# Kernel optimization log

Hardware: AMD Instinct MI355X
Metric: run time of the kernel (lower is better)

The kernel has to match this reference:

```python
import jax, jax.numpy as jnp
import numpy as np

H, HD = 8, 32            # num_heads, head_dim
OUT = H * HD             # out_channels = 256
NUM_GRAPHS = 1


def segment_softmax(logits, seg, num_segments):
    m = jax.ops.segment_max(logits, seg, num_segments=num_segments)
    m = jnp.where(jnp.isfinite(m), m, 0.0)
    e = jnp.exp(logits - m[seg])
    s = jax.ops.segment_sum(e, seg, num_segments=num_segments)
    return e / (s[seg] + 1e-16)


def setup_inputs():
    key = jax.random.key(0)
    ks = jax.random.split(key, 16)
    N, E, IN = 30000, 600000, 128
    s = 0.05
    return {
        "x": jax.random.normal(ks[0], (N, IN), jnp.float32),
        "edge_index": jax.random.randint(ks[1], (2, E), 0, N, jnp.int32),
        "edge_attr": jax.random.normal(ks[2], (E,), jnp.float32),
        "batch": jnp.zeros((N,), jnp.int32),
        # per-head GATConv params (stacked over heads)
        "W": jax.random.normal(ks[3], (H, IN, HD), jnp.float32) * s,
        "a_src": jax.random.normal(ks[4], (H, HD), jnp.float32) * s,
        "a_dst": jax.random.normal(ks[5], (H, HD), jnp.float32) * s,
        "conv_b": jnp.zeros((H, HD), jnp.float32),
        # shared fc (used twice in forward)
        "fc_w": jax.random.normal(ks[6], (OUT, OUT), jnp.float32) * s,
        "fc_b": jnp.zeros((OUT,), jnp.float32),
        "ln_w": jnp.ones((OUT,), jnp.float32),
        "ln_b": jnp.zeros((OUT,), jnp.float32),
        "gate_w": jax.random.normal(ks[7], (1, OUT), jnp.float32) * s,
        "gate_b": jnp.zeros((1,), jnp.float32),
        "gfc_w": jax.random.normal(ks[8], (OUT, OUT), jnp.float32) * s,
        "gfc_b": jnp.zeros((OUT,), jnp.float32),
    }


def reference(x, edge_index, edge_attr, batch, W, a_src, a_dst, conv_b,
              fc_w, fc_b, ln_w, ln_b, gate_w, gate_b, gfc_w, gfc_b):
    N = x.shape[0]
    # (dropout p=0.2 is identity in eval mode)
    # --- multi-head GATConv (heads=1 each, vectorized over H); PyG default
    # add_self_loops=True; edge_dim=None so edge_attr is ignored by the conv.
    loops = jnp.arange(N, dtype=edge_index.dtype)
    src = jnp.concatenate([edge_index[0], loops])  # [Etot]
    dst = jnp.concatenate([edge_index[1], loops])
    xp = jnp.einsum('ni,hid->nhd', x, W)                    # [N,H,HD]
    alpha_src = jnp.sum(xp * a_src[None], axis=-1)          # [N,H]
    alpha_dst = jnp.sum(xp * a_dst[None], axis=-1)          # [N,H]
    logits = jax.nn.leaky_relu(alpha_src[src] + alpha_dst[dst], 0.2)  # [Etot,H]
    alpha = segment_softmax(logits, dst, N)                 # [Etot,H]
    msg = alpha[:, :, None] * xp[src]                        # [Etot,H,HD]
    out = jax.ops.segment_sum(msg, dst, num_segments=N) + conv_b[None]
    x_local = out.reshape(N, OUT)                            # concat over heads
    # --- dense re-attention / softmax fusion
    sa = jax.nn.softmax(jax.nn.leaky_relu(x_local @ fc_w.T + fc_b, 0.01), axis=-1)
    x_local = jax.nn.leaky_relu(x_local * sa, 0.2)
    x_local = x_local @ fc_w.T + fc_b
    # LayerNorm (eps=1e-5)
    mu = jnp.mean(x_local, axis=-1, keepdims=True)
    var = jnp.mean(jnp.square(x_local - mu), axis=-1, keepdims=True)
    x_local = (x_local - mu) / jnp.sqrt(var + 1e-5) * ln_w + ln_b
    # F.normalize(p=2, dim=1)
    nrm = jnp.sqrt(jnp.sum(jnp.square(x_local), axis=1, keepdims=True))
    x_local = x_local / jnp.maximum(nrm, 1e-12)
    # --- GlobalAttention pooling
    gate = (x_local @ gate_w.T + gate_b)[:, 0]               # [N]
    g = segment_softmax(gate, batch, NUM_GRAPHS)             # [N]
    x_global = jax.ops.segment_sum(g[:, None] * x_local, batch,
                                   num_segments=NUM_GRAPHS)  # [1,OUT]
    ga = jax.nn.softmax(jax.nn.relu(x_global @ gfc_w.T + gfc_b), axis=-1)
    return x_local * ga[batch]                               # [N,OUT]
```

## Files before the change

kernel.cpp:

```cpp
#include <hip/hip_runtime.h>


#define PAD 64
#define CSTR 16

typedef __attribute__((ext_vector_type(8))) short bf16x8;
typedef __attribute__((ext_vector_type(4))) float f32x4;

__device__ __forceinline__ float leaky_f(float v, float s) { return v > 0.f ? v : s * v; }
__device__ __forceinline__ unsigned short f2bf(float f) {
  unsigned int u = __float_as_uint(f);
  u += 0x7fffu + ((u >> 16) & 1u);
  return (unsigned short)(u >> 16);
}
__device__ __forceinline__ float bf2f(unsigned short u) {
  return __uint_as_float(((unsigned int)u) << 16);
}
__device__ __forceinline__ float bf_lo(unsigned int u) {
  return __uint_as_float(u << 16);
}
__device__ __forceinline__ float bf_hi(unsigned int u) {
  return __uint_as_float(u & 0xffff0000u);
}
__device__ __forceinline__ float red16_sum(float v) {
#pragma unroll
  for (int m = 1; m < 16; m <<= 1) v += __shfl_xor(v, m);
  return v;
}
__device__ __forceinline__ float red16_max(float v) {
#pragma unroll
  for (int m = 1; m < 16; m <<= 1) v = fmaxf(v, __shfl_xor(v, m));
  return v;
}

__global__ void repack_zero_kernel(const float* __restrict__ W, const float* __restrict__ fc_w,
                                   const float* __restrict__ gfc_w,
                                   unsigned short* __restrict__ Wb,
                                   unsigned short* __restrict__ fcB, float* __restrict__ gfcT,
                                   int* __restrict__ count, int n) {
  int i = blockIdx.x * 256 + threadIdx.x;
  if (i < 256 * 128) {
    int c = i >> 7, k = i & 127;
    Wb[i] = f2bf(W[((c >> 5) * 128 + k) * 32 + (c & 31)]);
  } else if (i < 256 * 128 + 256 * 256) {
    int j = i - 256 * 128;
    fcB[j] = f2bf(fc_w[j]);
  } else if (i < 256 * 128 + 2 * 256 * 256) {
    int j = i - 256 * 128 - 256 * 256;
    gfcT[j] = gfc_w[(j & 255) * 256 + (j >> 8)];
  }
  if (i < n) count[i * CSTR] = 0;
}

template <int A_BF16>
__device__ __forceinline__ void gemm_body_64x256(
    const void* __restrict__ Av, const unsigned short* __restrict__ B,
    int row0, int n_rows, int K, short As[64][72], short Bs[256][72],
    f32x4 acc[4][4]) {
  int t = threadIdx.x;
  int wave = t >> 6, lane = t & 63;
  int m16 = lane & 15, quad = lane >> 4;
  int wc = wave * 64;
  for (int k0 = 0; k0 < K; k0 += 64) {
    if (A_BF16) {
      const unsigned short* A = (const unsigned short*)Av;
#pragma unroll
      for (int p = 0; p < 2; ++p) {
        int e = (p * 256 + t) * 8;
        int row = e >> 6, k = e & 63;
        int ar = row0 + row; if (ar > n_rows - 1) ar = n_rows - 1;
        uint4 q = *(const uint4*)(A + (size_t)ar * K + k0 + k);
        *(uint4*)&As[row][k] = q;
      }
    } else {
      const float* A = (const float*)Av;
#pragma unroll
      for (int p = 0; p < 4; ++p) {
        int e = (p * 256 + t) * 4;
        int row = e >> 6, k = e & 63;
        int ar = row0 + row; if (ar > n_rows - 1) ar = n_rows - 1;
        float4 q = *(const float4*)(A + (size_t)ar * K + k0 + k);
        unsigned int lo = (unsigned int)f2bf(q.x) | ((unsigned int)f2bf(q.y) << 16);
        unsigned int hi = (unsigned int)f2bf(q.z) | ((unsigned int)f2bf(q.w) << 16);
        *(uint2*)&As[row][k] = make_uint2(lo, hi);
      }
    }
#pragma unroll
    for (int p = 0; p < 8; ++p) {
      int e = (p * 256 + t) * 8;
      int nn = e >> 6, k = e & 63;
      uint4 q = *(const uint4*)(B + (size_t)nn * K + k0 + k);
      *(uint4*)&Bs[nn][k] = q;
    }
    __syncthreads();
#pragma unroll
    for (int ks = 0; ks < 64; ks += 32) {
      bf16x8 af[4], bfr[4];
#pragma unroll
      for (int i = 0; i < 4; ++i)
        af[i] = *(const bf16x8*)&As[i * 16 + m16][ks + quad * 8];
#pragma unroll
      for (int j = 0; j < 4; ++j)
        bfr[j] = *(const bf16x8*)&Bs[wc + j * 16 + m16][ks + quad * 8];
#pragma unroll
      for (int i = 0; i < 4; ++i)
#pragma unroll
        for (int j = 0; j < 4; ++j)
          acc[i][j] = __builtin_amdgcn_mfma_f32_16x16x32_bf16(af[i], bfr[j], acc[i][j], 0, 0, 0);
    }
    __syncthreads();
  }
}

__global__ __launch_bounds__(256) void gemm_xp_scatter(
    const float* __restrict__ A, const unsigned short* __restrict__ B,
    const float* __restrict__ a_src, const float* __restrict__ a_dst,
    unsigned short* __restrict__ xpb, float* __restrict__ asrc,
    float* __restrict__ adst, int n_rows,
    const int* __restrict__ esrc, const int* __restrict__ edst,
    int* __restrict__ count, unsigned short* __restrict__ ssrc, int E,
    int scat_blocks) {
  __shared__ short As[64][72];
  __shared__ short Bs[256][72];
  if ((int)blockIdx.x < scat_blocks) {
    int base = ((int)blockIdx.x * 256 + threadIdx.x) * 4;
    if (base + 4 <= E) {
      int4 d4 = *(const int4*)(edst + base);
      int4 s4 = *(const int4*)(esrc + base);
      int p0 = atomicAdd(&count[d4.x * CSTR], 1);
      int p1 = atomicAdd(&count[d4.y * CSTR], 1);
      int p2 = atomicAdd(&count[d4.z * CSTR], 1);
      int p3 = atomicAdd(&count[d4.w * CSTR], 1);
      if (p0 < PAD) ssrc[(size_t)d4.x * PAD + p0] = (unsigned short)s4.x;
      if (p1 < PAD) ssrc[(size_t)d4.y * PAD + p1] = (unsigned short)s4.y;
      if (p2 < PAD) ssrc[(size_t)d4.z * PAD + p2] = (unsigned short)s4.z;
      if (p3 < PAD) ssrc[(size_t)d4.w * PAD + p3] = (unsigned short)s4.w;
    } else {
      for (int i = base; i < E; ++i) {
        int d = edst[i];
        int p = atomicAdd(&count[d * CSTR], 1);
        if (p < PAD) ssrc[(size_t)d * PAD + p] = (unsigned short)esrc[i];
      }
    }
    return;
  }
  int t = threadIdx.x;
  int wave = t >> 6, lane = t & 63;
  int m16 = lane & 15, quad = lane >> 4;
  int wc = wave * 64;
  int row0 = ((int)blockIdx.x - scat_blocks) * 64;
  f32x4 acc[4][4];
#pragma unroll
  for (int i = 0; i < 4; ++i)
#pragma unroll
    for (int j = 0; j < 4; ++j) acc[i][j] = (f32x4){0.f, 0.f, 0.f, 0.f};
  gemm_body_64x256<0>(A, B, row0, n_rows, 128, As, Bs, acc);

  float av[4], bd[4];
#pragma unroll
  for (int j = 0; j < 4; ++j) {
    int c = wc + j * 16 + m16;
    av[j] = a_src[c];
    bd[j] = a_dst[c];
  }
#pragma unroll
  for (int i = 0; i < 4; ++i)
#pragma unroll
    for (int v = 0; v < 4; ++v) {
      int r = row0 + i * 16 + quad * 4 + v;
      if (r < n_rows) {
#pragma unroll
        for (int j = 0; j < 4; ++j)
          xpb[(size_t)r * 256 + wc + j * 16 + m16] = f2bf(acc[i][j][v]);
      }
      float s0 = acc[i][0][v] * av[0] + acc[i][1][v] * av[1];
      float s1 = acc[i][2][v] * av[2] + acc[i][3][v] * av[3];
      float d0 = acc[i][0][v] * bd[0] + acc[i][1][v] * bd[1];
      float d1 = acc[i][2][v] * bd[2] + acc[i][3][v] * bd[3];
      s0 = red16_sum(s0); s1 = red16_sum(s1);
      d0 = red16_sum(d0); d1 = red16_sum(d1);
      if (m16 == 0 && r < n_rows) {
        asrc[(size_t)r * 8 + 2 * wave] = s0;
        asrc[(size_t)r * 8 + 2 * wave + 1] = s1;
        adst[(size_t)r * 8 + 2 * wave] = d0;
        adst[(size_t)r * 8 + 2 * wave + 1] = d1;
      }
    }
}

__global__ __launch_bounds__(256) void agg_kernel(
    const unsigned short* __restrict__ xpb, const float* __restrict__ asrc,
    const float* __restrict__ adst, const int* __restrict__ count,
    const unsigned short* __restrict__ ssrc, const float* __restrict__ conv_b,
    unsigned short* __restrict__ xlocb, int n_nodes) {
  int t = threadIdx.x;
  int lane = t & 63;
  int hl = lane & 31;
  int half = lane >> 5;
  int wv = t >> 6;
  int n = blockIdx.x * 8 + wv * 2 + half;
  bool active = n < n_nodes;
  int nn = active ? n : 0;
  int hc = hl >> 2;
  int hp = hl & 7;
  int up = hl >> 3;
  int srcbase = (half << 5) + hc;

  float ad_p = adst[nn * 8 + hp];
  float ad_c = adst[nn * 8 + hc];

  float p = __expf(leaky_f(asrc[nn * 8 + hc] + ad_c, 0.2f));
  uint4 q = *(const uint4*)(xpb + (size_t)nn * 256 + hl * 8);
  float acc[8];
  acc[0] = p * bf_lo(q.x); acc[1] = p * bf_hi(q.x);
  acc[2] = p * bf_lo(q.y); acc[3] = p * bf_hi(q.y);
  acc[4] = p * bf_lo(q.z); acc[5] = p * bf_hi(q.z);
  acc[6] = p * bf_lo(q.w); acc[7] = p * bf_hi(q.w);
  float ssum = p;

  int beg = nn * PAD;
  int end = beg + (active ? count[nn * CSTR] : 0);
  int j = beg;
  for (; j + 4 <= end; j += 4) {
    ushort4 s4 = *(const ushort4*)(ssrc + j);
    int svp = (up & 1) ? ((up & 2) ? s4.w : s4.y) : ((up & 2) ? s4.z : s4.x);
    float pp = __expf(leaky_f(asrc[svp * 8 + hp] + ad_p, 0.2f));
    uint4 q0 = *(const uint4*)(xpb + (size_t)s4.x * 256 + hl * 8);
    uint4 q1 = *(const uint4*)(xpb + (size_t)s4.y * 256 + hl * 8);
    uint4 q2 = *(const uint4*)(xpb + (size_t)s4.z * 256 + hl * 8);
    uint4 q3 = *(const uint4*)(xpb + (size_t)s4.w * 256 + hl * 8);
    float p0 = __shfl(pp, srcbase);
    float p1 = __shfl(pp, srcbase + 8);
    float p2 = __shfl(pp, srcbase + 16);
    float p3 = __shfl(pp, srcbase + 24);
    acc[0] += p0 * bf_lo(q0.x); acc[1] += p0 * bf_hi(q0.x);
    acc[2] += p0 * bf_lo(q0.y); acc[3] += p0 * bf_hi(q0.y);
    acc[4] += p0 * bf_lo(q0.z); acc[5] += p0 * bf_hi(q0.z);
    acc[6] += p0 * bf_lo(q0.w); acc[7] += p0 * bf_hi(q0.w);
    acc[0] += p1 * bf_lo(q1.x); acc[1] += p1 * bf_hi(q1.x);
    acc[2] += p1 * bf_lo(q1.y); acc[3] += p1 * bf_hi(q1.y);
    acc[4] += p1 * bf_lo(q1.z); acc[5] += p1 * bf_hi(q1.z);
    acc[6] += p1 * bf_lo(q1.w); acc[7] += p1 * bf_hi(q1.w);
    acc[0] += p2 * bf_lo(q2.x); acc[1] += p2 * bf_hi(q2.x);
    acc[2] += p2 * bf_lo(q2.y); acc[3] += p2 * bf_hi(q2.y);
    acc[4] += p2 * bf_lo(q2.z); acc[5] += p2 * bf_hi(q2.z);
    acc[6] += p2 * bf_lo(q2.w); acc[7] += p2 * bf_hi(q2.w);
    acc[0] += p3 * bf_lo(q3.x); acc[1] += p3 * bf_hi(q3.x);
    acc[2] += p3 * bf_lo(q3.y); acc[3] += p3 * bf_hi(q3.y);
    acc[4] += p3 * bf_lo(q3.z); acc[5] += p3 * bf_hi(q3.z);
    acc[6] += p3 * bf_lo(q3.w); acc[7] += p3 * bf_hi(q3.w);
    ssum += p0 + p1 + p2 + p3;
  }
  for (; j < end; ++j) {
    int sv = ssrc[j];
    float p1 = __expf(leaky_f(asrc[sv * 8 + hc] + ad_c, 0.2f));
    uint4 q1 = *(const uint4*)(xpb + (size_t)sv * 256 + hl * 8);
    acc[0] += p1 * bf_lo(q1.x); acc[1] += p1 * bf_hi(q1.x);
    acc[2] += p1 * bf_lo(q1.y); acc[3] += p1 * bf_hi(q1.y);
    acc[4] += p1 * bf_lo(q1.z); acc[5] += p1 * bf_hi(q1.z);
    acc[6] += p1 * bf_lo(q1.w); acc[7] += p1 * bf_hi(q1.w);
    ssum += p1;
  }
  if (!active) return;
  float inv = 1.f / (ssum + 1e-16f);
  float4 b0 = *(const float4*)(conv_b + hl * 8);
  float4 b1 = *(const float4*)(conv_b + hl * 8 + 4);
  unsigned int w0 = (unsigned int)f2bf(acc[0] * inv + b0.x) |
                    ((unsigned int)f2bf(acc[1] * inv + b0.y) << 16);
  unsigned int w1 = (unsigned int)f2bf(acc[2] * inv + b0.z) |
                    ((unsigned int)f2bf(acc[3] * inv + b0.w) << 16);
  unsigned int w2 = (unsigned int)f2bf(acc[4] * inv + b1.x) |
                    ((unsigned int)f2bf(acc[5] * inv + b1.y) << 16);
  unsigned int w3 = (unsigned int)f2bf(acc[6] * inv + b1.z) |
                    ((unsigned int)f2bf(acc[7] * inv + b1.w) << 16);
  *(uint4*)(xlocb + (size_t)n * 256 + hl * 8) = make_uint4(w0, w1, w2, w3);
}

__global__ __launch_bounds__(256) void gemm_sm(
    const unsigned short* __restrict__ A, const unsigned short* __restrict__ B,
    const float* __restrict__ bias, unsigned short* __restrict__ x2b, int n_rows) {
  __shared__ short As[64][72];
  __shared__ short Bs[256][72];
  __shared__ float red[4][64];
  __shared__ float rowv[64];
  int t = threadIdx.x;
  int wave = t >> 6, lane = t & 63;
  int m16 = lane & 15, quad = lane >> 4;
  int wc = wave * 64;
  int row0 = blockIdx.x * 64;
  f32x4 acc[4][4];
#pragma unroll
  for (int i = 0; i < 4; ++i)
#pragma unroll
    for (int j = 0; j < 4; ++j) acc[i][j] = (f32x4){0.f, 0.f, 0.f, 0.f};
  gemm_body_64x256<1>(A, B, row0, n_rows, 256, As, Bs, acc);

  float bvv[4];
#pragma unroll
  for (int j = 0; j < 4; ++j) bvv[j] = bias[wc + j * 16 + m16];
#pragma unroll
  for (int i = 0; i < 4; ++i)
#pragma unroll
    for (int j = 0; j < 4; ++j)
#pragma unroll
      for (int v = 0; v < 4; ++v)
        acc[i][j][v] = leaky_f(acc[i][j][v] + bvv[j], 0.01f);

  float M[4][4];
#pragma unroll
  for (int i = 0; i < 4; ++i)
#pragma unroll
    for (int v = 0; v < 4; ++v) {
      float m = fmaxf(fmaxf(acc[i][0][v], acc[i][1][v]), fmaxf(acc[i][2][v], acc[i][3][v]));
      M[i][v] = red16_max(m);
    }
  if (m16 == 0)
#pragma unroll
    for (int i = 0; i < 4; ++i)
#pragma unroll
      for (int v = 0; v < 4; ++v) red[wave][i * 16 + quad * 4 + v] = M[i][v];
  __syncthreads();
  if (t < 64) rowv[t] = fmaxf(fmaxf(red[0][t], red[1][t]), fmaxf(red[2][t], red[3][t]));
  __syncthreads();
#pragma unroll
  for (int i = 0; i < 4; ++i)
#pragma unroll
    for (int v = 0; v < 4; ++v) M[i][v] = rowv[i * 16 + quad * 4 + v];
  __syncthreads();

  float S[4][4];
#pragma unroll
  for (int i = 0; i < 4; ++i)
#pragma unroll
    for (int v = 0; v < 4; ++v) {
#pragma unroll
      for (int j = 0; j < 4; ++j) acc[i][j][v] = __expf(acc[i][j][v] - M[i][v]);
      float s = acc[i][0][v] + acc[i][1][v] + acc[i][2][v] + acc[i][3][v];
      S[i][v] = red16_sum(s);
    }
  if (m16 == 0)
#pragma unroll
    for (int i = 0; i < 4; ++i)
#pragma unroll
      for (int v = 0; v < 4; ++v) red[wave][i * 16 + quad * 4 + v] = S[i][v];
  __syncthreads();
  if (t < 64) rowv[t] = red[0][t] + red[1][t] + red[2][t] + red[3][t];
  __syncthreads();

#pragma unroll
  for (int i = 0; i < 4; ++i)
#pragma unroll
    for (int v = 0; v < 4; ++v) {
      int r = row0 + i * 16 + quad * 4 + v;
      float inv = 1.f / rowv[i * 16 + quad * 4 + v];
      if (r < n_rows) {
#pragma unroll
        for (int j = 0; j < 4; ++j) {
          int c = wc + j * 16 + m16;
          float xv = bf2f(A[(size_t)r * 256 + c]);
          x2b[(size_t)r * 256 + c] = f2bf(leaky_f(xv * acc[i][j][v] * inv, 0.2f));
        }
      }
    }
}

__global__ __launch_bounds__(256) void gemm_ln(
    const unsigned short* __restrict__ A, const unsigned short* __restrict__ B,
    const float* __restrict__ bias, const float* __restrict__ ln_w,
    const float* __restrict__ ln_b, const float* __restrict__ gate_w,
    const float* __restrict__ gate_b, unsigned short* __restrict__ Cout,
    float* __restrict__ pooled, float* __restrict__ pooledS, int n_rows) {
  __shared__ short As[64][72];
  __shared__ short Bs[256][72];
  __shared__ float red[4][64];
  __shared__ float rowv[64];
  __shared__ float eg[64];
  int t = threadIdx.x;
  int wave = t >> 6, lane = t & 63;
  int m16 = lane & 15, quad = lane >> 4;
  int wc = wave * 64;
  int row0 = blockIdx.x * 64;
  f32x4 acc[4][4];
#pragma unroll
  for (int i = 0; i < 4; ++i)
#pragma unroll
    for (int j = 0; j < 4; ++j) acc[i][j] = (f32x4){0.f, 0.f, 0.f, 0.f};
  gemm_body_64x256<1>(A, B, row0, n_rows, 256, As, Bs, acc);

  float bvv[4], lw[4], lb[4], gw[4];
#pragma unroll
  for (int j = 0; j < 4; ++j) {
    int c = wc + j * 16 + m16;
    bvv[j] = bias[c]; lw[j] = ln_w[c]; lb[j] = ln_b[c]; gw[j] = gate_w[c];
  }
#pragma unroll
  for (int i = 0; i < 4; ++i)
#pragma unroll
    for (int j = 0; j < 4; ++j)
#pragma unroll
      for (int v = 0; v < 4; ++v) acc[i][j][v] += bvv[j];

  float MU[4][4];
#pragma unroll
  for (int i = 0; i < 4; ++i)
#pragma unroll
    for (int v = 0; v < 4; ++v)
      MU[i][v] = red16_sum(acc[i][0][v] + acc[i][1][v] + acc[i][2][v] + acc[i][3][v]);
  if (m16 == 0)
#pragma unroll
    for (int i = 0; i < 4; ++i)
#pragma unroll
      for (int v = 0; v < 4; ++v) red[wave][i * 16 + quad * 4 + v] = MU[i][v];
  __syncthreads();
  if (t < 64) rowv[t] = (red[0][t] + red[1][t] + red[2][t] + red[3][t]) * (1.f / 256.f);
  __syncthreads();
#pragma unroll
  for (int i = 0; i < 4; ++i)
#pragma unroll
    for (int v = 0; v < 4; ++v) MU[i][v] = rowv[i * 16 + quad * 4 + v];
  __syncthreads();
#pragma unroll
  for (int i = 0; i < 4; ++i)
#pragma unroll
    for (int j = 0; j < 4; ++j)
#pragma unroll
      for (int v = 0; v < 4; ++v) acc[i][j][v] -= MU[i][v];

  float RS[4][4];
#pragma unroll
  for (int i = 0; i < 4; ++i)
#pragma unroll
    for (int v = 0; v < 4; ++v) {
      float q = acc[i][0][v] * acc[i][0][v] + acc[i][1][v] * acc[i][1][v] +
                acc[i][2][v] * acc[i][2][v] + acc[i][3][v] * acc[i][3][v];
      RS[i][v] = red16_sum(q);
    }
  if (m16 == 0)
#pragma unroll
    for (int i = 0; i < 4; ++i)
#pragma unroll
      for (int v = 0; v < 4; ++v) red[wave][i * 16 + quad * 4 + v] = RS[i][v];
  __syncthreads();
  if (t < 64)
    rowv[t] = rsqrtf((red[0][t] + red[1][t] + red[2][t] + red[3][t]) * (1.f / 256.f) + 1e-5f);
  __syncthreads();
#pragma unroll
  for (int i = 0; i < 4; ++i)
#pragma unroll
    for (int v = 0; v < 4; ++v) RS[i][v] = rowv[i * 16 + quad * 4 + v];
  __syncthreads();
#pragma unroll
  for (int i = 0; i < 4; ++i)
#pragma unroll
    for (int j = 0; j < 4; ++j)
#pragma unroll
      for (int v = 0; v < 4; ++v)
        acc[i][j][v] = acc[i][j][v] * RS[i][v] * lw[j] + lb[j];

  float NV[4][4];
#pragma unroll
  for (int i = 0; i < 4; ++i)
#pragma unroll
    for (int v = 0; v < 4; ++v) {
      float q = acc[i][0][v] * acc[i][0][v] + acc[i][1][v] * acc[i][1][v] +
                acc[i][2][v] * acc[i][2][v] + acc[i][3][v] * acc[i][3][v];
      NV[i][v] = red16_sum(q);
    }
  if (m16 == 0)
#pragma unroll
    for (int i = 0; i < 4; ++i)
#pragma unroll
      for (int v = 0; v < 4; ++v) red[wave][i * 16 + quad * 4 + v] = NV[i][v];
  __syncthreads();
  if (t < 64)
    rowv[t] = 1.f / fmaxf(sqrtf(red[0][t] + red[1][t] + red[2][t] + red[3][t]), 1e-12f);
  __syncthreads();
#pragma unroll
  for (int i = 0; i < 4; ++i)
#pragma unroll
    for (int v = 0; v < 4; ++v) NV[i][v] = rowv[i * 16 + quad * 4 + v];
  __syncthreads();
#pragma unroll
  for (int i = 0; i < 4; ++i)
#pragma unroll
    for (int j = 0; j < 4; ++j)
#pragma unroll
      for (int v = 0; v < 4; ++v) acc[i][j][v] *= NV[i][v];

  float GP[4][4];
#pragma unroll
  for (int i = 0; i < 4; ++i)
#pragma unroll
    for (int v = 0; v < 4; ++v) {
      float g = acc[i][0][v] * gw[0] + acc[i][1][v] * gw[1] +
                acc[i][2][v] * gw[2] + acc[i][3][v] * gw[3];
      GP[i][v] = red16_sum(g);
    }
  if (m16 == 0)
#pragma unroll
    for (int i = 0; i < 4; ++i)
#pragma unroll
      for (int v = 0; v < 4; ++v) red[wave][i * 16 + quad * 4 + v] = GP[i][v];
  __syncthreads();
  if (t < 64) {
    float gp = red[0][t] + red[1][t] + red[2][t] + red[3][t];
    float e = (row0 + t < n_rows) ? __expf(gp + gate_b[0]) : 0.f;
    eg[t] = e;
#pragma unroll
    for (int m = 1; m < 64; m <<= 1) e += __shfl_xor(e, m);
    if (t == 0) pooledS[blockIdx.x] = e;
  }
  __syncthreads();

  {
    float pt[4] = {0.f, 0.f, 0.f, 0.f};
#pragma unroll
    for (int i = 0; i < 4; ++i)
#pragma unroll
      for (int v = 0; v < 4; ++v) {
        float w = eg[i * 16 + quad * 4 + v];
#pragma unroll
        for (int j = 0; j < 4; ++j) pt[j] += w * acc[i][j][v];
      }
#pragma unroll
    for (int j = 0; j < 4; ++j) {
      float sj = pt[j];
      sj += __shfl_xor(sj, 16);
      sj += __shfl_xor(sj, 32);
      if (quad == 0) pooled[(size_t)blockIdx.x * 256 + wc + j * 16 + m16] = sj;
    }
  }

#pragma unroll
  for (int i = 0; i < 4; ++i)
#pragma unroll
    for (int v = 0; v < 4; ++v) {
      int r = row0 + i * 16 + quad * 4 + v;
      if (r < n_rows) {
#pragma unroll
        for (int j = 0; j < 4; ++j)
          Cout[(size_t)r * 256 + wc + j * 16 + m16] = f2bf(acc[i][j][v]);
      }
    }
}

__global__ __launch_bounds__(1024) void finalize_gfc(
    const float* __restrict__ pooled, const float* __restrict__ pooledS, int nb,
    const float* __restrict__ gfcT, const float* __restrict__ gfc_b,
    float* __restrict__ ga) {
  __shared__ float sm[1024];
  __shared__ float xs[256];
  __shared__ float av[256];
  int t = threadIdx.x, c = t & 255, part = t >> 8;
  float s = 0.f;
  for (int b = t; b < nb; b += 1024) s += pooledS[b];
  sm[t] = s;
  __syncthreads();
  for (int st = 512; st > 0; st >>= 1) {
    if (t < st) sm[t] += sm[t + st];
    __syncthreads();
  }
  float S = sm[0];
  __syncthreads();
  float xc = 0.f;
#pragma unroll 4
  for (int b = part; b < nb; b += 4) xc += pooled[(size_t)b * 256 + c];
  sm[t] = xc;
  __syncthreads();
  if (part == 0) xs[c] = (sm[c] + sm[c + 256] + sm[c + 512] + sm[c + 768]) / (S + 1e-16f);
  __syncthreads();
  float a = 0.f;
  for (int i = part * 64; i < part * 64 + 64; ++i) a += xs[i] * gfcT[i * 256 + c];
  sm[t] = a;
  __syncthreads();
  if (part == 0)
    av[c] = fmaxf(sm[c] + sm[c + 256] + sm[c + 512] + sm[c + 768] + gfc_b[c], 0.f);
  __syncthreads();
  sm[t] = (t < 256) ? av[t] : -1e30f;
  __syncthreads();
  for (int st = 512; st > 0; st >>= 1) {
    if (t < st) sm[t] = fmaxf(sm[t], sm[t + st]);
    __syncthreads();
  }
  float m = sm[0];
  __syncthreads();
  if (part == 0) av[c] = __expf(av[c] - m);
  __syncthreads();
  sm[t] = (t < 256) ? av[t] : 0.f;
  __syncthreads();
  for (int st = 512; st > 0; st >>= 1) {
    if (t < st) sm[t] += sm[t + st];
    __syncthreads();
  }
  if (part == 0) ga[c] = av[c] / sm[0];
}

__global__ void out_kernel(const ushort4* __restrict__ xlb4, const float4* __restrict__ ga4,
                           float4* __restrict__ out4, int total4) {
  int i = blockIdx.x * 256 + threadIdx.x;
  if (i >= total4) return;
  ushort4 q = xlb4[i];
  float4 g = ga4[i & 63];
  float4 v;
  v.x = bf2f(q.x) * g.x; v.y = bf2f(q.y) * g.y;
  v.z = bf2f(q.z) * g.z; v.w = bf2f(q.w) * g.w;
  out4[i] = v;
}

extern "C" void kernel_launch(void* const* d_in, const int* in_sizes, int n_in,
                              void* d_out, int out_size, void* d_ws, size_t ws_size,
                              hipStream_t stream) {
  const float* x      = (const float*)d_in[0];
  const int* edge_idx = (const int*)d_in[1];
  const float* W      = (const float*)d_in[4];
  const float* a_src  = (const float*)d_in[5];
  const float* a_dst  = (const float*)d_in[6];
  const float* conv_b = (const float*)d_in[7];
  const float* fc_w   = (const float*)d_in[8];
  const float* fc_b   = (const float*)d_in[9];
  const float* ln_w   = (const float*)d_in[10];
  const float* ln_b   = (const float*)d_in[11];
  const float* gate_w = (const float*)d_in[12];
  const float* gate_b = (const float*)d_in[13];
  const float* gfc_w  = (const float*)d_in[14];
  const float* gfc_b  = (const float*)d_in[15];
  (void)n_in; (void)out_size; (void)ws_size;

  int N = in_sizes[0] / 128;
  int E = in_sizes[1] / 2;
  const int* src = edge_idx;
  const int* dst = edge_idx + E;

  char* p = (char*)d_ws;
  auto alloc = [&](size_t bytes) -> char* {
    char* r = p;
    p += (bytes + 255) & ~(size_t)255;
    return r;
  };
  int g64 = (N + 63) / 64;
  unsigned short* xlocb = (unsigned short*)alloc((size_t)N * 256 * 2);
  unsigned short* xpb  = (unsigned short*)alloc((size_t)N * 256 * 2);
  unsigned short* x2b  = (unsigned short*)alloc((size_t)N * 256 * 2);
  unsigned short* xlb  = (unsigned short*)alloc((size_t)N * 256 * 2);
  float* asrc  = (float*)alloc((size_t)N * 8 * 4);
  float* adst  = (float*)alloc((size_t)N * 8 * 4);
  unsigned short* Wb   = (unsigned short*)alloc(256 * 128 * 2);
  unsigned short* fcB  = (unsigned short*)alloc(256 * 256 * 2);
  float* gfcT  = (float*)alloc(256 * 256 * 4);
  int*   count = (int*)alloc((size_t)N * CSTR * 4);
  unsigned short* ssrc = (unsigned short*)alloc((size_t)N * PAD * 2);
  float* pooled  = (float*)alloc((size_t)g64 * 256 * 4);
  float* pooledS = (float*)alloc((size_t)g64 * 4);
  float* ga    = (float*)alloc(1024);

  int eb4 = (E + 1023) / 1024;

  repack_zero_kernel<<<(256 * 128 + 2 * 256 * 256 + 255) / 256, 256, 0, stream>>>(
      W, fc_w, gfc_w, Wb, fcB, gfcT, count, N);
  gemm_xp_scatter<<<eb4 + g64, 256, 0, stream>>>(
      x, Wb, a_src, a_dst, xpb, asrc, adst, N, src, dst, count, ssrc, E, eb4);
  agg_kernel<<<(N + 7) / 8, 256, 0, stream>>>(
      xpb, asrc, adst, count, ssrc, conv_b, xlocb, N);
  gemm_sm<<<g64, 256, 0, stream>>>(xlocb, fcB, fc_b, x2b, N);
  gemm_ln<<<g64, 256, 0, stream>>>(x2b, fcB, fc_b, ln_w, ln_b, gate_w, gate_b,
                                   xlb, pooled, pooledS, N);
  finalize_gfc<<<1, 1024, 0, stream>>>(pooled, pooledS, g64, gfcT, gfc_b, ga);
  out_kernel<<<(N * 64 + 255) / 256, 256, 0, stream>>>(
      (const ushort4*)xlb, (const float4*)ga, (float4*)d_out, N * 64);
}
```

Baseline: 248.3 us.

## Fuse softmax-reattention GEMM with LayerNorm GEMM and prefetch neighbor indices in aggregation

Merges the two fc GEMM kernels into one. The whole 64x256 row tile of the aggregated features stays in shared memory, and the reattention output is rewritten in place, so the intermediate x2b buffer is never written to or read back from global memory and one launch goes away. The aggregation loop also software-prefetches the next group of four source indices and their attention logits, which shortens the dependent load chain. The cost is a larger shared-memory footprint per block (about 33KB for X2 plus Bs), which may lower occupancy.

```diff
diff --git a/kernel.cpp b/kernel.cpp
--- a/kernel.cpp
+++ b/kernel.cpp
@@ -31,6 +31,9 @@
 #pragma unroll
   for (int m = 1; m < 16; m <<= 1) v = fmaxf(v, __shfl_xor(v, m));
   return v;
+}
+__device__ __forceinline__ int pick4(ushort4 s, int up) {
+  return (up & 1) ? ((up & 2) ? s.w : s.y) : ((up & 2) ? s.z : s.x);
 }
 
 __global__ void repack_zero_kernel(const float* __restrict__ W, const float* __restrict__ fc_w,
@@ -52,9 +55,8 @@
   if (i < n) count[i * CSTR] = 0;
 }
 
-template <int A_BF16>
-__device__ __forceinline__ void gemm_body_64x256(
-    const void* __restrict__ Av, const unsigned short* __restrict__ B,
+__device__ __forceinline__ void gemm_body_f32(
+    const float* __restrict__ A, const unsigned short* __restrict__ B,
     int row0, int n_rows, int K, short As[64][72], short Bs[256][72],
     f32x4 acc[4][4]) {
   int t = threadIdx.x;
@@ -62,28 +64,15 @@
   int m16 = lane & 15, quad = lane >> 4;
   int wc = wave * 64;
   for (int k0 = 0; k0 < K; k0 += 64) {
-    if (A_BF16) {
-      const unsigned short* A = (const unsigned short*)Av;
-#pragma unroll
-      for (int p = 0; p < 2; ++p) {
-        int e = (p * 256 + t) * 8;
-        int row = e >> 6, k = e & 63;
-        int ar = row0 + row; if (ar > n_rows - 1) ar = n_rows - 1;
-        uint4 q = *(const uint4*)(A + (size_t)ar * K + k0 + k);
-        *(uint4*)&As[row][k] = q;
-      }
-    } else {
-      const float* A = (const float*)Av;
-#pragma unroll
-      for (int p = 0; p < 4; ++p) {
-        int e = (p * 256 + t) * 4;
-        int row = e >> 6, k = e & 63;
-        int ar = row0 + row; if (ar > n_rows - 1) ar = n_rows - 1;
-        float4 q = *(const float4*)(A + (size_t)ar * K + k0 + k);
-        unsigned int lo = (unsigned int)f2bf(q.x) | ((unsigned int)f2bf(q.y) << 16);
-        unsigned int hi = (unsigned int)f2bf(q.z) | ((unsigned int)f2bf(q.w) << 16);
-        *(uint2*)&As[row][k] = make_uint2(lo, hi);
-      }
+#pragma unroll
+    for (int p = 0; p < 4; ++p) {
+      int e = (p * 256 + t) * 4;
+      int row = e >> 6, k = e & 63;
+      int ar = row0 + row; if (ar > n_rows - 1) ar = n_rows - 1;
+      float4 q = *(const float4*)(A + (size_t)ar * K + k0 + k);
+      unsigned int lo = (unsigned int)f2bf(q.x) | ((unsigned int)f2bf(q.y) << 16);
+      unsigned int hi = (unsigned int)f2bf(q.z) | ((unsigned int)f2bf(q.w) << 16);
+      *(uint2*)&As[row][k] = make_uint2(lo, hi);
     }
 #pragma unroll
     for (int p = 0; p < 8; ++p) {
@@ -154,7 +143,7 @@
   for (int i = 0; i < 4; ++i)
 #pragma unroll
     for (int j = 0; j < 4; ++j) acc[i][j] = (f32x4){0.f, 0.f, 0.f, 0.f};
-  gemm_body_64x256<0>(A, B, row0, n_rows, 128, As, Bs, acc);
+  gemm_body_f32(A, B, row0, n_rows, 128, As, Bs, acc);
 
   float av[4], bd[4];
 #pragma unroll
@@ -218,38 +207,45 @@
   acc[6] = p * bf_lo(q.w); acc[7] = p * bf_hi(q.w);
   float ssum = p;
 
+  int cnt = active ? count[nn * CSTR] : 0;
   int beg = nn * PAD;
-  int end = beg + (active ? count[nn * CSTR] : 0);
+  int end = beg + cnt;
+  int jend = beg + (cnt & ~3);
   int j = beg;
-  for (; j + 4 <= end; j += 4) {
+  if (j < jend) {
     ushort4 s4 = *(const ushort4*)(ssrc + j);
-    int svp = (up & 1) ? ((up & 2) ? s4.w : s4.y) : ((up & 2) ? s4.z : s4.x);
-    float pp = __expf(leaky_f(asrc[svp * 8 + hp] + ad_p, 0.2f));
-    uint4 q0 = *(const uint4*)(xpb + (size_t)s4.x * 256 + hl * 8);
-    uint4 q1 = *(const uint4*)(xpb + (size_t)s4.y * 256 + hl * 8);
-    uint4 q2 = *(const uint4*)(xpb + (size_t)s4.z * 256 + hl * 8);
-    uint4 q3 = *(const uint4*)(xpb + (size_t)s4.w * 256 + hl * 8);
-    float p0 = __shfl(pp, srcbase);
-    float p1 = __shfl(pp, srcbase + 8);
-    float p2 = __shfl(pp, srcbase + 16);
-    float p3 = __shfl(pp, srcbase + 24);
-    acc[0] += p0 * bf_lo(q0.x); acc[1] += p0 * bf_hi(q0.x);
-    acc[2] += p0 * bf_lo(q0.y); acc[3] += p0 * bf_hi(q0.y);
-    acc[4] += p0 * bf_lo(q0.z); acc[5] += p0 * bf_hi(q0.z);
-    acc[6] += p0 * bf_lo(q0.w); acc[7] += p0 * bf_hi(q0.w);
-    acc[0] += p1 * bf_lo(q1.x); acc[1] += p1 * bf_hi(q1.x);
-    acc[2] += p1 * bf_lo(q1.y); acc[3] += p1 * bf_hi(q1.y);
-    acc[4] += p1 * bf_lo(q1.z); acc[5] += p1 * bf_hi(q1.z);
-    acc[6] += p1 * bf_lo(q1.w); acc[7] += p1 * bf_hi(q1.w);
-    acc[0] += p2 * bf_lo(q2.x); acc[1] += p2 * bf_hi(q2.x);
-    acc[2] += p2 * bf_lo(q2.y); acc[3] += p2 * bf_hi(q2.y);
-    acc[4] += p2 * bf_lo(q2.z); acc[5] += p2 * bf_hi(q2.z);
-    acc[6] += p2 * bf_lo(q2.w); acc[7] += p2 * bf_hi(q2.w);
-    acc[0] += p3 * bf_lo(q3.x); acc[1] += p3 * bf_hi(q3.x);
-    acc[2] += p3 * bf_lo(q3.y); acc[3] += p3 * bf_hi(q3.y);
-    acc[4] += p3 * bf_lo(q3.z); acc[5] += p3 * bf_hi(q3.z);
-    acc[6] += p3 * bf_lo(q3.w); acc[7] += p3 * bf_hi(q3.w);
-    ssum += p0 + p1 + p2 + p3;
+    float a_cur = asrc[pick4(s4, up) * 8 + hp];
+    for (; j < jend; j += 4) {
+      ushort4 s4n = (j + 4 < jend) ? *(const ushort4*)(ssrc + j + 4) : s4;
+      uint4 q0 = *(const uint4*)(xpb + (size_t)s4.x * 256 + hl * 8);
+      uint4 q1 = *(const uint4*)(xpb + (size_t)s4.y * 256 + hl * 8);
+      uint4 q2 = *(const uint4*)(xpb + (size_t)s4.z * 256 + hl * 8);
+      uint4 q3 = *(const uint4*)(xpb + (size_t)s4.w * 256 + hl * 8);
+      float pp = __expf(leaky_f(a_cur + ad_p, 0.2f));
+      float a_nxt = asrc[pick4(s4n, up) * 8 + hp];
+      float p0 = __shfl(pp, srcbase);
+      float p1 = __shfl(pp, srcbase + 8);
+      float p2 = __shfl(pp, srcbase + 16);
+      float p3 = __shfl(pp, srcbase + 24);
+      acc[0] += p0 * bf_lo(q0.x); acc[1] += p0 * bf_hi(q0.x);
+      acc[2] += p0 * bf_lo(q0.y); acc[3] += p0 * bf_hi(q0.y);
+      acc[4] += p0 * bf_lo(q0.z); acc[5] += p0 * bf_hi(q0.z);
+      acc[6] += p0 * bf_lo(q0.w); acc[7] += p0 * bf_hi(q0.w);
+      acc[0] += p1 * bf_lo(q1.x); acc[1] += p1 * bf_hi(q1.x);
+      acc[2] += p1 * bf_lo(q1.y); acc[3] += p1 * bf_hi(q1.y);
+      acc[4] += p1 * bf_lo(q1.z); acc[5] += p1 * bf_hi(q1.z);
+      acc[6] += p1 * bf_lo(q1.w); acc[7] += p1 * bf_hi(q1.w);
+      acc[0] += p2 * bf_lo(q2.x); acc[1] += p2 * bf_hi(q2.x);
+      acc[2] += p2 * bf_lo(q2.y); acc[3] += p2 * bf_hi(q2.y);
+      acc[4] += p2 * bf_lo(q2.z); acc[5] += p2 * bf_hi(q2.z);
+      acc[6] += p2 * bf_lo(q2.w); acc[7] += p2 * bf_hi(q2.w);
+      acc[0] += p3 * bf_lo(q3.x); acc[1] += p3 * bf_hi(q3.x);
+      acc[2] += p3 * bf_lo(q3.y); acc[3] += p3 * bf_hi(q3.y);
+      acc[4] += p3 * bf_lo(q3.z); acc[5] += p3 * bf_hi(q3.z);
+      acc[6] += p3 * bf_lo(q3.w); acc[7] += p3 * bf_hi(q3.w);
+      ssum += p0 + p1 + p2 + p3;
+      s4 = s4n; a_cur = a_nxt;
+    }
   }
   for (; j < end; ++j) {
     int sv = ssrc[j];
@@ -276,101 +272,13 @@
   *(uint4*)(xlocb + (size_t)n * 256 + hl * 8) = make_uint4(w0, w1, w2, w3);
 }
 
-__global__ __launch_bounds__(256) void gemm_sm(
-    const unsigned short* __restrict__ A, const unsigned short* __restrict__ B,
-    const float* __restrict__ bias, unsigned short* __restrict__ x2b, int n_rows) {
-  __shared__ short As[64][72];
-  __shared__ short Bs[256][72];
-  __shared__ float red[4][64];
-  __shared__ float rowv[64];
-  int t = threadIdx.x;
-  int wave = t >> 6, lane = t & 63;
-  int m16 = lane & 15, quad = lane >> 4;
-  int wc = wave * 64;
-  int row0 = blockIdx.x * 64;
-  f32x4 acc[4][4];
-#pragma unroll
-  for (int i = 0; i < 4; ++i)
-#pragma unroll
-    for (int j = 0; j < 4; ++j) acc[i][j] = (f32x4){0.f, 0.f, 0.f, 0.f};
-  gemm_body_64x256<1>(A, B, row0, n_rows, 256, As, Bs, acc);
-
-  float bvv[4];
-#pragma unroll
-  for (int j = 0; j < 4; ++j) bvv[j] = bias[wc + j * 16 + m16];
-#pragma unroll
-  for (int i = 0; i < 4; ++i)
-#pragma unroll
-    for (int j = 0; j < 4; ++j)
-#pragma unroll
-      for (int v = 0; v < 4; ++v)
-        acc[i][j][v] = leaky_f(acc[i][j][v] + bvv[j], 0.01f);
-
-  float M[4][4];
-#pragma unroll
-  for (int i = 0; i < 4; ++i)
-#pragma unroll
-    for (int v = 0; v < 4; ++v) {
-      float m = fmaxf(fmaxf(acc[i][0][v], acc[i][1][v]), fmaxf(acc[i][2][v], acc[i][3][v]));
-      M[i][v] = red16_max(m);
-    }
-  if (m16 == 0)
-#pragma unroll
-    for (int i = 0; i < 4; ++i)
-#pragma unroll
-      for (int v = 0; v < 4; ++v) red[wave][i * 16 + quad * 4 + v] = M[i][v];
-  __syncthreads();
-  if (t < 64) rowv[t] = fmaxf(fmaxf(red[0][t], red[1][t]), fmaxf(red[2][t], red[3][t]));
-  __syncthreads();
-#pragma unroll
-  for (int i = 0; i < 4; ++i)
-#pragma unroll
-    for (int v = 0; v < 4; ++v) M[i][v] = rowv[i * 16 + quad * 4 + v];
-  __syncthreads();
-
-  float S[4][4];
-#pragma unroll
-  for (int i = 0; i < 4; ++i)
-#pragma unroll
-    for (int v = 0; v < 4; ++v) {
-#pragma unroll
-      for (int j = 0; j < 4; ++j) acc[i][j][v] = __expf(acc[i][j][v] - M[i][v]);
-      float s = acc[i][0][v] + acc[i][1][v] + acc[i][2][v] + acc[i][3][v];
-      S[i][v] = red16_sum(s);
-    }
-  if (m16 == 0)
-#pragma unroll
-    for (int i = 0; i < 4; ++i)
-#pragma unroll
-      for (int v = 0; v < 4; ++v) red[wave][i * 16 + quad * 4 + v] = S[i][v];
-  __syncthreads();
-  if (t < 64) rowv[t] = red[0][t] + red[1][t] + red[2][t] + red[3][t];
-  __syncthreads();
-
-#pragma unroll
-  for (int i = 0; i < 4; ++i)
-#pragma unroll
-    for (int v = 0; v < 4; ++v) {
-      int r = row0 + i * 16 + quad * 4 + v;
-      float inv = 1.f / rowv[i * 16 + quad * 4 + v];
-      if (r < n_rows) {
-#pragma unroll
-        for (int j = 0; j < 4; ++j) {
-          int c = wc + j * 16 + m16;
-          float xv = bf2f(A[(size_t)r * 256 + c]);
-          x2b[(size_t)r * 256 + c] = f2bf(leaky_f(xv * acc[i][j][v] * inv, 0.2f));
-        }
-      }
-    }
-}
-
-__global__ __launch_bounds__(256) void gemm_ln(
+__global__ __launch_bounds__(256) void gemm_sm_ln(
     const unsigned short* __restrict__ A, const unsigned short* __restrict__ B,
     const float* __restrict__ bias, const float* __restrict__ ln_w,
     const float* __restrict__ ln_b, const float* __restrict__ gate_w,
     const float* __restrict__ gate_b, unsigned short* __restrict__ Cout,
     float* __restrict__ pooled, float* __restrict__ pooledS, int n_rows) {
-  __shared__ short As[64][72];
+  __shared__ short X2[64][260];
   __shared__ short Bs[256][72];
   __shared__ float red[4][64];
   __shared__ float rowv[64];
@@ -380,14 +288,147 @@
   int m16 = lane & 15, quad = lane >> 4;
   int wc = wave * 64;
   int row0 = blockIdx.x * 64;
+
+#pragma unroll
+  for (int p = 0; p < 8; ++p) {
+    int e = (p * 256 + t) * 8;
+    int row = e >> 8, col = e & 255;
+    int ar = row0 + row; if (ar > n_rows - 1) ar = n_rows - 1;
+    uint4 qv = *(const uint4*)(A + (size_t)ar * 256 + col);
+    *(uint4*)&X2[row][col] = qv;
+  }
+
   f32x4 acc[4][4];
 #pragma unroll
   for (int i = 0; i < 4; ++i)
 #pragma unroll
     for (int j = 0; j < 4; ++j) acc[i][j] = (f32x4){0.f, 0.f, 0.f, 0.f};
-  gemm_body_64x256<1>(A, B, row0, n_rows, 256, As, Bs, acc);
-
-  float bvv[4], lw[4], lb[4], gw[4];
+
+  for (int k0 = 0; k0 < 256; k0 += 64) {
+#pragma unroll
+    for (int p = 0; p < 8; ++p) {
+      int e = (p * 256 + t) * 8;
+      int nn = e >> 6, k = e & 63;
+      uint4 qv = *(const uint4*)(B + (size_t)nn * 256 + k0 + k);
+      *(uint4*)&Bs[nn][k] = qv;
+    }
+    __syncthreads();
+#pragma unroll
+    for (int ks = 0; ks < 64; ks += 32) {
+      bf16x8 af[4], bfr[4];
+#pragma unroll
+      for (int i = 0; i < 4; ++i)
+        af[i] = *(const bf16x8*)&X2[i * 16 + m16][k0 + ks + quad * 8];
+#pragma unroll
+      for (int j = 0; j < 4; ++j)
+        bfr[j] = *(const bf16x8*)&Bs[wc + j * 16 + m16][ks + quad * 8];
+#pragma unroll
+      for (int i = 0; i < 4; ++i)
+#pragma unroll
+        for (int j = 0; j < 4; ++j)
+          acc[i][j] = __builtin_amdgcn_mfma_f32_16x16x32_bf16(af[i], bfr[j], acc[i][j], 0, 0, 0);
+    }
+    __syncthreads();
+  }
+
+  float bvv[4];
+#pragma unroll
+  for (int j = 0; j < 4; ++j) bvv[j] = bias[wc + j * 16 + m16];
+#pragma unroll
+  for (int i = 0; i < 4; ++i)
+#pragma unroll
+    for (int j = 0; j < 4; ++j)
+#pragma unroll
+      for (int v = 0; v < 4; ++v)
+        acc[i][j][v] = leaky_f(acc[i][j][v] + bvv[j], 0.01f);
+
+  float M[4][4];
+#pragma unroll
+  for (int i = 0; i < 4; ++i)
+#pragma unroll
+    for (int v = 0; v < 4; ++v) {
+      float m = fmaxf(fmaxf(acc[i][0][v], acc[i][1][v]), fmaxf(acc[i][2][v], acc[i][3][v]));
+      M[i][v] = red16_max(m);
+    }
+  if (m16 == 0)
+#pragma unroll
+    for (int i = 0; i < 4; ++i)
+#pragma unroll
+      for (int v = 0; v < 4; ++v) red[wave][i * 16 + quad * 4 + v] = M[i][v];
+  __syncthreads();
+  if (t < 64) rowv[t] = fmaxf(fmaxf(red[0][t], red[1][t]), fmaxf(red[2][t], red[3][t]));
+  __syncthreads();
+#pragma unroll
+  for (int i = 0; i < 4; ++i)
+#pragma unroll
+    for (int v = 0; v < 4; ++v) M[i][v] = rowv[i * 16 + quad * 4 + v];
+  __syncthreads();
+
+  float S[4][4];
+#pragma unroll
+  for (int i = 0; i < 4; ++i)
+#pragma unroll
+    for (int v = 0; v < 4; ++v) {
+#pragma unroll
+      for (int j = 0; j < 4; ++j) acc[i][j][v] = __expf(acc[i][j][v] - M[i][v]);
+      float s = acc[i][0][v] + acc[i][1][v] + acc[i][2][v] + acc[i][3][v];
+      S[i][v] = red16_sum(s);
+    }
+  if (m16 == 0)
+#pragma unroll
+    for (int i = 0; i < 4; ++i)
+#pragma unroll
+      for (int v = 0; v < 4; ++v) red[wave][i * 16 + quad * 4 + v] = S[i][v];
+  __syncthreads();
+  if (t < 64) rowv[t] = red[0][t] + red[1][t] + red[2][t] + red[3][t];
+  __syncthreads();
+
+#pragma unroll
+  for (int i = 0; i < 4; ++i)
+#pragma unroll
+    for (int v = 0; v < 4; ++v) {
+      int rl = i * 16 + quad * 4 + v;
+      float inv = 1.f / rowv[rl];
+#pragma unroll
+      for (int j = 0; j < 4; ++j) {
+        int c = wc + j * 16 + m16;
+        float xv = bf2f((unsigned short)X2[rl][c]);
+        X2[rl][c] = (short)f2bf(leaky_f(xv * acc[i][j][v] * inv, 0.2f));
+      }
+    }
+
+#pragma unroll
+  for (int i = 0; i < 4; ++i)
+#pragma unroll
+    for (int j = 0; j < 4; ++j) acc[i][j] = (f32x4){0.f, 0.f, 0.f, 0.f};
+  for (int k0 = 0; k0 < 256; k0 += 64) {
+#pragma unroll
+    for (int p = 0; p < 8; ++p) {
+      int e = (p * 256 + t) * 8;
+      int nn = e >> 6, k = e & 63;
+      uint4 qv = *(const uint4*)(B + (size_t)nn * 256 + k0 + k);
+      *(uint4*)&Bs[nn][k] = qv;
+    }
+    __syncthreads();
+#pragma unroll
+    for (int ks = 0; ks < 64; ks += 32) {
+      bf16x8 af[4], bfr[4];
+#pragma unroll
+      for (int i = 0; i < 4; ++i)
+        af[i] = *(const bf16x8*)&X2[i * 16 + m16][k0 + ks + quad * 8];
+#pragma unroll
+      for (int j = 0; j < 4; ++j)
+        bfr[j] = *(const bf16x8*)&Bs[wc + j * 16 + m16][ks + quad * 8];
+#pragma unroll
+      for (int i = 0; i < 4; ++i)
+#pragma unroll
+        for (int j = 0; j < 4; ++j)
+          acc[i][j] = __builtin_amdgcn_mfma_f32_16x16x32_bf16(af[i], bfr[j], acc[i][j], 0, 0, 0);
+    }
+    __syncthreads();
+  }
+
+  float lw[4], lb[4], gw[4];
 #pragma unroll
   for (int j = 0; j < 4; ++j) {
     int c = wc + j * 16 + m16;
@@ -431,9 +472,9 @@
   for (int i = 0; i < 4; ++i)
 #pragma unroll
     for (int v = 0; v < 4; ++v) {
-      float q = acc[i][0][v] * acc[i][0][v] + acc[i][1][v] * acc[i][1][v] +
-                acc[i][2][v] * acc[i][2][v] + acc[i][3][v] * acc[i][3][v];
-      RS[i][v] = red16_sum(q);
+      float qq = acc[i][0][v] * acc[i][0][v] + acc[i][1][v] * acc[i][1][v] +
+                 acc[i][2][v] * acc[i][2][v] + acc[i][3][v] * acc[i][3][v];
+      RS[i][v] = red16_sum(qq);
     }
   if (m16 == 0)
 #pragma unroll
@@ -462,9 +503,9 @@
   for (int i = 0; i < 4; ++i)
 #pragma unroll
     for (int v = 0; v < 4; ++v) {
-      float q = acc[i][0][v] * acc[i][0][v] + acc[i][1][v] * acc[i][1][v] +
-                acc[i][2][v] * acc[i][2][v] + acc[i][3][v] * acc[i][3][v];
-      NV[i][v] = red16_sum(q);
+      float qq = acc[i][0][v] * acc[i][0][v] + acc[i][1][v] * acc[i][1][v] +
+                 acc[i][2][v] * acc[i][2][v] + acc[i][3][v] * acc[i][3][v];
+      NV[i][v] = red16_sum(qq);
     }
   if (m16 == 0)
 #pragma unroll
@@ -640,7 +681,6 @@
   int g64 = (N + 63) / 64;
   unsigned short* xlocb = (unsigned short*)alloc((size_t)N * 256 * 2);
   unsigned short* xpb  = (unsigned short*)alloc((size_t)N * 256 * 2);
-  unsigned short* x2b  = (unsigned short*)alloc((size_t)N * 256 * 2);
   unsigned short* xlb  = (unsigned short*)alloc((size_t)N * 256 * 2);
   float* asrc  = (float*)alloc((size_t)N * 8 * 4);
   float* adst  = (float*)alloc((size_t)N * 8 * 4);
@@ -661,9 +701,8 @@
       x, Wb, a_src, a_dst, xpb, asrc, adst, N, src, dst, count, ssrc, E, eb4);
   agg_kernel<<<(N + 7) / 8, 256, 0, stream>>>(
       xpb, asrc, adst, count, ssrc, conv_b, xlocb, N);
-  gemm_sm<<<g64, 256, 0, stream>>>(xlocb, fcB, fc_b, x2b, N);
-  gemm_ln<<<g64, 256, 0, stream>>>(x2b, fcB, fc_b, ln_w, ln_b, gate_w, gate_b,
-                                   xlb, pooled, pooledS, N);
+  gemm_sm_ln<<<g64, 256, 0, stream>>>(xlocb, fcB, fc_b, ln_w, ln_b, gate_w,
+                                      gate_b, xlb, pooled, pooledS, N);
   finalize_gfc<<<1, 1024, 0, stream>>>(pooled, pooledS, g64, gfcT, gfc_b, ga);
   out_kernel<<<(N * 64 + 255) / 256, 256, 0, stream>>>(
       (const ushort4*)xlb, (const float4*)ga, (float4*)d_out, N * 64);
```

Result: no change. 248.9 us (+0.2%).
